# Performance work log

Hardware: AMD Instinct MI355X
Metric: run time of the kernel (lower is better)

Reference implementation:

```python
import jax, jax.numpy as jnp
import numpy as np

SOS = 1

def setup_inputs() -> dict:
    key = jax.random.key(0)
    ks = jax.random.split(key, 12)
    B, S, T, H, V = 64, 128, 32, 1024, 32000
    sc = 0.02
    return {
        'encoder_outputs': jax.random.normal(ks[0], (B, S, H), jnp.float32),
        'encoder_hidden': jax.random.normal(ks[1], (1, B, H), jnp.float32),
        'target_tensor': jax.random.randint(ks[2], (B, T), 0, V),
        'embedding': jax.random.normal(ks[3], (V, H), jnp.float32) * sc,
        'Wa': jax.random.normal(ks[4], (H, H), jnp.float32) * sc,
        'ba': jnp.zeros((H,), jnp.float32),
        'Ua': jax.random.normal(ks[5], (H, H), jnp.float32) * sc,
        'bu': jnp.zeros((H,), jnp.float32),
        'Va': jax.random.normal(ks[6], (1, H), jnp.float32) * sc,
        'bv': jnp.zeros((1,), jnp.float32),
        'W_ih': jax.random.normal(ks[7], (3 * H, 2 * H), jnp.float32) * sc,
        'b_ih': jnp.zeros((3 * H,), jnp.float32),
        'W_hh': jax.random.normal(ks[8], (3 * H, H), jnp.float32) * sc,
        'b_hh': jnp.zeros((3 * H,), jnp.float32),
        'W_out': jax.random.normal(ks[9], (V, H), jnp.float32) * sc,
        'b_out': jnp.zeros((V,), jnp.float32),
    }

def reference(encoder_outputs, encoder_hidden, target_tensor, embedding,
              Wa, ba, Ua, bu, Va, bv, W_ih, b_ih, W_hh, b_hh, W_out, b_out):
    B, S, H = encoder_outputs.shape
    T = target_tensor.shape[1]
    # teacher forcing: input at step i is SOS for i=0 else target[:, i-1]
    tokens = jnp.concatenate([jnp.full((B, 1), SOS, target_tensor.dtype),
                              target_tensor[:, :-1]], axis=1)  # (B,T)
    emb = embedding[tokens]  # (B,T,H); dropout is identity (eval)
    keys_proj = jnp.einsum('bsh,gh->bsg', encoder_outputs, Ua) + bu  # Ua(keys), (B,S,H)
    h0 = encoder_hidden[0]  # (B,H)

    def step(h, x_t):
        # Bahdanau attention: Va(tanh(Wa q + Ua k))
        q = h @ Wa.T + ba  # (B,H)
        scores = jnp.einsum('bsh,h->bs', jnp.tanh(q[:, None, :] + keys_proj), Va[0]) + bv[0]
        w = jax.nn.softmax(scores, axis=-1)  # (B,S)
        ctx = jnp.einsum('bs,bsh->bh', w, encoder_outputs)
        x = jnp.concatenate([x_t, ctx], axis=-1)  # (B,2H)
        # GRU cell (PyTorch convention)
        gi = x @ W_ih.T + b_ih
        gh = h @ W_hh.T + b_hh
        ir, iz, inn = jnp.split(gi, 3, axis=-1)
        hr, hz, hn = jnp.split(gh, 3, axis=-1)
        r = jax.nn.sigmoid(ir + hr)
        z = jax.nn.sigmoid(iz + hz)
        n = jnp.tanh(inn + r * hn)
        h_new = (1.0 - z) * n + z * h
        logits = h_new @ W_out.T + b_out  # (B,V)
        return h_new, (logits, w)

    h_final, (logits, weights) = jax.lax.scan(step, h0, jnp.swapaxes(emb, 0, 1))
    log_probs = jax.nn.log_softmax(jnp.swapaxes(logits, 0, 1), axis=-1)  # (B,T,V)
    attentions = jnp.swapaxes(weights, 0, 1)  # (B,T,S)
    return log_probs, h_final[None], attentions
```

## Files before the change

### kernel.cpp

```cpp
#include <hip/hip_runtime.h>


typedef unsigned short u16;
typedef __bf16 bf16x8 __attribute__((ext_vector_type(8)));
typedef float f32x4 __attribute__((ext_vector_type(4)));
typedef u16 u16x8 __attribute__((ext_vector_type(8)));

#define DEV __device__ __forceinline__

DEV u16 f2b(float f) {
  union { float f; unsigned u; } v; v.f = f;
  unsigned r = v.u + 0x7fffu + ((v.u >> 16) & 1u);
  return (u16)(r >> 16);
}
DEV float b2f(u16 b) {
  union { unsigned u; float f; } v; v.u = ((unsigned)b) << 16;
  return v.f;
}
DEV float sigm(float x) { return 1.f / (1.f + __expf(-x)); }
DEV float ftanh(float x) {
  x = fminf(fmaxf(x, -20.f), 20.f);
  float e = __expf(2.f * x);
  return (e - 1.f) / (e + 1.f);
}
DEV void gl16(const void* g, void* l) {
  __builtin_amdgcn_global_load_lds((const __attribute__((address_space(1))) void*)g,
                                   (__attribute__((address_space(3))) void*)l, 16, 0, 0);
}

__global__ __launch_bounds__(256) void cvtall(const float* __restrict__ enc, const float* __restrict__ Ua,
                                              const float* __restrict__ Wa, const float* __restrict__ Whh,
                                              const float* __restrict__ Wout, u16* __restrict__ enc_b,
                                              u16* __restrict__ Ua_b, u16* __restrict__ Wa_b,
                                              u16* __restrict__ Whh_b, u16* __restrict__ Wout_b) {
  const long q_enc = 2097152;
  const long q_ua = q_enc + 262144;
  const long q_wa = q_ua + 262144;
  const long q_whh = q_wa + 786432;
  const long total = q_whh + 8192000;
  long stride = (long)gridDim.x * 256;
  for (long i = (long)blockIdx.x * 256 + threadIdx.x; i < total; i += stride) {
    const float* src; u16* dst; long off;
    if (i < q_enc) { src = enc; dst = enc_b; off = i; }
    else if (i < q_ua) { src = Ua; dst = Ua_b; off = i - q_enc; }
    else if (i < q_wa) { src = Wa; dst = Wa_b; off = i - q_ua; }
    else if (i < q_whh) { src = Whh; dst = Whh_b; off = i - q_wa; }
    else { src = Wout; dst = Wout_b; off = i - q_whh; }
    float4 v = ((const float4*)src)[off];
    ushort4 o; o.x = f2b(v.x); o.y = f2b(v.y); o.z = f2b(v.z); o.w = f2b(v.w);
    ((ushort4*)dst)[off] = o;
  }
}

__global__ __launch_bounds__(256) void cvtsplitk(const float* __restrict__ in, u16* __restrict__ o1,
                                                 u16* __restrict__ o2) {
  const long n4 = (long)3072 * 2048 / 4;
  long stride = (long)gridDim.x * 256;
  for (long i = (long)blockIdx.x * 256 + threadIdx.x; i < n4; i += stride) {
    long e = i * 4;
    int row = (int)(e >> 11), col = (int)(e & 2047);
    float4 v = ((const float4*)in)[i];
    ushort4 o; o.x = f2b(v.x); o.y = f2b(v.y); o.z = f2b(v.z); o.w = f2b(v.w);
    u16* dst = (col < 1024) ? (o1 + (size_t)row * 1024 + col) : (o2 + (size_t)row * 1024 + col - 1024);
    *(ushort4*)dst = o;
  }
}

__global__ __launch_bounds__(256) void embk(const float* __restrict__ embd, const int* __restrict__ tgt,
                                            u16* __restrict__ out) {
  int i = blockIdx.x * 256 + threadIdx.x;
  size_t e = (size_t)i * 4;
  int h = (int)(e & 1023);
  int bt = (int)(e >> 10);
  int b = bt >> 5, t = bt & 31;
  int tok = (t == 0) ? 1 : tgt[b * 32 + t - 1];
  const float* src = embd + (size_t)tok * 1024 + h;
  ushort4 o; o.x = f2b(src[0]); o.y = f2b(src[1]); o.z = f2b(src[2]); o.w = f2b(src[3]);
  *(ushort4*)(out + e) = o;
}

__global__ __launch_bounds__(256) void hinitk(const float* __restrict__ eh, float* __restrict__ hf,
                                              u16* __restrict__ hb) {
  int i = blockIdx.x * 256 + threadIdx.x;
  float v = eh[i];
  hf[i] = v; hb[i] = f2b(v);
}

template <int MODE>
__global__ __launch_bounds__(256) void gemm_tile(const u16* __restrict__ A, const u16* __restrict__ Bm,
                                                 const float* __restrict__ bias, float* __restrict__ Cf,
                                                 u16* __restrict__ Cb, int K, int ldc, int nTM) {
  __shared__ __attribute__((aligned(16))) u16 As[128 * 32];
  __shared__ __attribute__((aligned(16))) u16 Bs[128 * 32];
  const int tid = threadIdx.x, lane = tid & 63, w = tid >> 6;
  const int chunk = gridDim.x >> 3, wg = blockIdx.x;
  const int id = (wg & 7) * chunk + (wg >> 3);
  const int m = id % nTM, n = id / nTM;
  const int m0 = m * 128, n0 = n * 128;
  const int wm = w >> 1, wn = w & 1;
  const int l16 = lane & 15, kg = lane >> 4;
  const int srow = lane >> 2;
  const int skk = (((lane & 3) ^ ((srow >> 1) & 3)) * 8);
  const int slot = (kg ^ ((l16 >> 1) & 3)) * 8;

  f32x4 acc[4][4];
#pragma unroll
  for (int i = 0; i < 4; ++i)
#pragma unroll
    for (int j = 0; j < 4; ++j) acc[i][j] = f32x4{0.f, 0.f, 0.f, 0.f};

  for (int k0 = 0; k0 < K; k0 += 32) {
#pragma unroll
    for (int ch = 0; ch < 2; ++ch) {
      int c = w + ch * 4;
      gl16(A + (size_t)(m0 + c * 16 + srow) * K + k0 + skk, &As[c * 512]);
      gl16(Bm + (size_t)(n0 + c * 16 + srow) * K + k0 + skk, &Bs[c * 512]);
    }
    __syncthreads();
    bf16x8 av[4], bv[4];
#pragma unroll
    for (int i = 0; i < 4; ++i) av[i] = *(const bf16x8*)&As[(wm * 4 + i) * 512 + l16 * 32 + slot];
#pragma unroll
    for (int j = 0; j < 4; ++j) bv[j] = *(const bf16x8*)&Bs[(wn * 4 + j) * 512 + l16 * 32 + slot];
#pragma unroll
    for (int i = 0; i < 4; ++i)
#pragma unroll
      for (int j = 0; j < 4; ++j)
        acc[i][j] = __builtin_amdgcn_mfma_f32_16x16x32_bf16(av[i], bv[j], acc[i][j], 0, 0, 0);
    __syncthreads();
  }
#pragma unroll
  for (int i = 0; i < 4; ++i) {
    int rowb = m0 + (wm * 4 + i) * 16 + kg * 4;
#pragma unroll
    for (int j = 0; j < 4; ++j) {
      int col = n0 + (wn * 4 + j) * 16 + l16;
      float bb = bias[col];
#pragma unroll
      for (int r = 0; r < 4; ++r) {
        int row = rowb + r;
        float v = acc[i][j][r] + bb;
        if (MODE == 0) Cf[(size_t)row * ldc + col] = v;
        else Cb[(size_t)row * ldc + col] = f2b(v);
      }
    }
  }
}

template <int MODE>
__global__ __launch_bounds__(256, 2) void gemm_wide(const u16* __restrict__ A, const u16* __restrict__ Bm,
                                                    const float* __restrict__ bias, float* __restrict__ Cf,
                                                    u16* __restrict__ Cb, int K, int ldc) {
  __shared__ __attribute__((aligned(16))) u16 As[128 * 32];
  __shared__ __attribute__((aligned(16))) u16 Bs[256 * 32];
  const int tid = threadIdx.x, lane = tid & 63, w = tid >> 6;
  const int chunk = gridDim.x >> 3, wg = blockIdx.x;
  const int id = (wg & 7) * chunk + (wg >> 3);
  const int r_ = id % 80;
  const int m = r_ & 15, n = 5 * (id / 80) + (r_ >> 4);
  const int m0 = m * 128, n0 = n * 256;
  const int wm = w >> 1, wn = w & 1;
  const int l16 = lane & 15, kg = lane >> 4;
  const int srow = lane >> 2;
  const int skk = (((lane & 3) ^ ((srow >> 1) & 3)) * 8);
  const int slot = (kg ^ ((l16 >> 1) & 3)) * 8;

  f32x4 acc[4][8];
#pragma unroll
  for (int i = 0; i < 4; ++i)
#pragma unroll
    for (int j = 0; j < 8; ++j) acc[i][j] = f32x4{0.f, 0.f, 0.f, 0.f};

  for (int k0 = 0; k0 < K; k0 += 32) {
#pragma unroll
    for (int ch = 0; ch < 2; ++ch) {
      int c = w + ch * 4;
      gl16(A + (size_t)(m0 + c * 16 + srow) * K + k0 + skk, &As[c * 512]);
    }
#pragma unroll
    for (int ch = 0; ch < 4; ++ch) {
      int c = w + ch * 4;
      gl16(Bm + (size_t)(n0 + c * 16 + srow) * K + k0 + skk, &Bs[c * 512]);
    }
    __syncthreads();
    bf16x8 av[4], bv[8];
#pragma unroll
    for (int i = 0; i < 4; ++i) av[i] = *(const bf16x8*)&As[(wm * 4 + i) * 512 + l16 * 32 + slot];
#pragma unroll
    for (int j = 0; j < 8; ++j) bv[j] = *(const bf16x8*)&Bs[(wn * 8 + j) * 512 + l16 * 32 + slot];
#pragma unroll
    for (int i = 0; i < 4; ++i)
#pragma unroll
      for (int j = 0; j < 8; ++j)
        acc[i][j] = __builtin_amdgcn_mfma_f32_16x16x32_bf16(av[i], bv[j], acc[i][j], 0, 0, 0);
    __syncthreads();
  }
#pragma unroll
  for (int i = 0; i < 4; ++i) {
    int rowb = m0 + (wm * 4 + i) * 16 + kg * 4;
#pragma unroll
    for (int j = 0; j < 8; ++j) {
      int col = n0 + (wn * 8 + j) * 16 + l16;
      float bb = bias[col];
#pragma unroll
      for (int r = 0; r < 4; ++r) {
        int row = rowb + r;
        float v = acc[i][j][r] + bb;
        int b_ = row & 63, t_ = row >> 6;
        size_t ro = ((size_t)b_ * 32 + t_) * ldc + col;
        if (MODE == 0) Cf[ro] = v; else Cb[ro] = f2b(v);
      }
    }
  }
}

__global__ __launch_bounds__(256) void qkghk(const u16* __restrict__ hb, const u16* __restrict__ W1,
                                             float* __restrict__ qghp) {
  const int tid = threadIdx.x, lane = tid & 63, w = tid >> 6;
  const int l16 = lane & 15, kg = lane >> 4;
  const int pg = blockIdx.x >> 2, ks = blockIdx.x & 3;
  const u16* ap = hb + (size_t)(w * 16 + l16) * 1024 + ks * 256 + kg * 8;
  const u16* bp = W1 + (size_t)(pg * 16 + l16) * 1024 + ks * 256 + kg * 8;
  f32x4 a = {0.f, 0.f, 0.f, 0.f};
#pragma unroll
  for (int k0 = 0; k0 < 256; k0 += 32)
    a = __builtin_amdgcn_mfma_f32_16x16x32_bf16(*(const bf16x8*)(ap + k0), *(const bf16x8*)(bp + k0),
                                                a, 0, 0, 0);
  const int col = pg * 16 + l16;
#pragma unroll
  for (int r = 0; r < 4; ++r) {
    int b = w * 16 + kg * 4 + r;
    qghp[(size_t)ks * 262144 + b * 4096 + col] = a[r];
  }
}

__global__ __launch_bounds__(256) void scorekq(const float* __restrict__ qghp, const float* __restrict__ ba,
                                               const float* __restrict__ Va, const u16* __restrict__ kp,
                                               float* __restrict__ sc) {
  const int b = blockIdx.x >> 2, sq = blockIdx.x & 3;
  const int tid = threadIdx.x, lane = tid & 63, w = tid >> 6;
  __shared__ float qs[1024], vas[1024];
#pragma unroll
  for (int j = 0; j < 4; ++j) {
    int e = tid + j * 256;
    qs[e] = qghp[b * 4096 + e] + qghp[262144 + b * 4096 + e] + qghp[524288 + b * 4096 + e] +
            qghp[786432 + b * 4096 + e] + ba[e];
    vas[e] = Va[e];
  }
  __syncthreads();
#pragma unroll
  for (int si = 0; si < 8; ++si) {
    int s = sq * 32 + w * 8 + si;
    const bf16x8* kv = (const bf16x8*)(kp + ((size_t)b * 128 + s) * 1024);
    float a = 0.f;
#pragma unroll
    for (int i2 = 0; i2 < 2; ++i2) {
      int e = lane + 64 * i2;
      bf16x8 k8 = kv[e];
#pragma unroll
      for (int j = 0; j < 8; ++j) a += vas[e * 8 + j] * ftanh(qs[e * 8 + j] + (float)k8[j]);
    }
#pragma unroll
    for (int off = 32; off; off >>= 1) a += __shfl_xor(a, off);
    if (lane == 0) sc[b * 128 + s] = a;
  }
}

__global__ __launch_bounds__(256) void wsumgate(const float* __restrict__ scb, const u16* __restrict__ encW2,
                                                const float* __restrict__ gie, const float* __restrict__ qghp,
                                                const float* __restrict__ bhh, float* __restrict__ hf,
                                                u16* __restrict__ hbW, u16* __restrict__ hall,
                                                float* __restrict__ hfin, float* __restrict__ att_out, int t) {
  const int b = blockIdx.x >> 2, cg = blockIdx.x & 3;
  const int tid = threadIdx.x, lane = tid & 63, w = tid >> 6;
  __shared__ float wsm[128];
  if (w == 0) {
    float v0 = scb[b * 128 + lane], v1 = scb[b * 128 + 64 + lane];
    float mx = fmaxf(v0, v1);
#pragma unroll
    for (int off = 32; off; off >>= 1) mx = fmaxf(mx, __shfl_xor(mx, off));
    float e0 = __expf(v0 - mx), e1 = __expf(v1 - mx);
    float sm = e0 + e1;
#pragma unroll
    for (int off = 32; off; off >>= 1) sm += __shfl_xor(sm, off);
    float inv = 1.f / sm;
    e0 *= inv; e1 *= inv;
    wsm[lane] = e0; wsm[lane + 64] = e1;
    if (cg == 0) {
      size_t ao = ((size_t)b * 32 + t) * 128;
      att_out[ao + lane] = e0;
      att_out[ao + lane + 64] = e1;
    }
  }
  __syncthreads();
  const int col = cg * 256 + tid;
  float a0 = 0.f, a1 = 0.f, a2 = 0.f;
  const u16* ep = encW2 + (size_t)b * 128 * 3072 + col;
#pragma unroll 8
  for (int s = 0; s < 128; ++s) {
    float ws = wsm[s];
    a0 += ws * b2f(ep[0]);
    a1 += ws * b2f(ep[1024]);
    a2 += ws * b2f(ep[2048]);
    ep += 3072;
  }
  const float* ge = gie + ((size_t)b * 32 + t) * 3072 + col;
  const float* qg = qghp + (size_t)b * 4096 + 1024 + col;
  float hr = qg[0] + qg[262144] + qg[524288] + qg[786432] + bhh[col];
  float hz = qg[1024] + qg[1024 + 262144] + qg[1024 + 524288] + qg[1024 + 786432] + bhh[col + 1024];
  float hn = qg[2048] + qg[2048 + 262144] + qg[2048 + 524288] + qg[2048 + 786432] + bhh[col + 2048];
  float rr = sigm(a0 + ge[0] + hr);
  float zz = sigm(a1 + ge[1024] + hz);
  float nn = ftanh(a2 + ge[2048] + rr * hn);
  const int i = b * 1024 + col;
  float hp = hf[i];
  float hv = (1.f - zz) * nn + zz * hp;
  hf[i] = hv;
  u16 h16 = f2b(hv);
  hbW[i] = h16;
  hall[((size_t)t * 64 + b) * 1024 + col] = h16;
  if (t == 31) hfin[i] = hv;
}

__global__ __launch_bounds__(256) void smaxctxk(const float* __restrict__ sc, const u16* __restrict__ encb,
                                                u16* __restrict__ ctxb, float* __restrict__ att_out, int t) {
  const int b = blockIdx.x >> 2, hq = blockIdx.x & 3;
  const int tid = threadIdx.x, lane = tid & 63, w = tid >> 6;
  __shared__ float wsm[128];
  if (w == 0) {
    float v0 = sc[b * 128 + lane], v1 = sc[b * 128 + 64 + lane];
    float mx = fmaxf(v0, v1);
#pragma unroll
    for (int off = 32; off; off >>= 1) mx = fmaxf(mx, __shfl_xor(mx, off));
    float e0 = __expf(v0 - mx), e1 = __expf(v1 - mx);
    float sm = e0 + e1;
#pragma unroll
    for (int off = 32; off; off >>= 1) sm += __shfl_xor(sm, off);
    float inv = 1.f / sm;
    e0 *= inv; e1 *= inv;
    wsm[lane] = e0; wsm[lane + 64] = e1;
    if (hq == 0) {
      size_t ao = ((size_t)b * 32 + t) * 128;
      att_out[ao + lane] = e0;
      att_out[ao + lane + 64] = e1;
    }
  }
  __syncthreads();
  const int h = hq * 256 + tid;
  const u16* ep = encb + (size_t)b * 131072 + h;
  float c = 0.f;
#pragma unroll 8
  for (int s = 0; s < 128; ++s) c += wsm[s] * b2f(ep[(size_t)s * 1024]);
  ctxb[(size_t)b * 1024 + h] = f2b(c);
}

__global__ __launch_bounds__(256) void gi2w(const u16* __restrict__ ctxb, const u16* __restrict__ Wih2,
                                            float* __restrict__ gic) {
  const int tid = threadIdx.x, lane = tid & 63, w = tid >> 6;
  const int l16 = lane & 15, kg = lane >> 4;
  const int c0 = blockIdx.x * 16;
  const u16* ap = ctxb + (size_t)(w * 16 + l16) * 1024 + kg * 8;
  const u16* bp = Wih2 + (size_t)(c0 + l16) * 1024 + kg * 8;
  f32x4 a0 = {0.f, 0.f, 0.f, 0.f}, a1 = {0.f, 0.f, 0.f, 0.f};
#pragma unroll 4
  for (int k0 = 0; k0 < 1024; k0 += 64) {
    a0 = __builtin_amdgcn_mfma_f32_16x16x32_bf16(*(const bf16x8*)(ap + k0), *(const bf16x8*)(bp + k0),
                                                 a0, 0, 0, 0);
    a1 = __builtin_amdgcn_mfma_f32_16x16x32_bf16(*(const bf16x8*)(ap + k0 + 32),
                                                 *(const bf16x8*)(bp + k0 + 32), a1, 0, 0, 0);
  }
  const int col = c0 + l16;
#pragma unroll
  for (int r = 0; r < 4; ++r) {
    int b = w * 16 + kg * 4 + r;
    gic[(size_t)b * 3072 + col] = a0[r] + a1[r];
  }
}

__global__ __launch_bounds__(256) void gatesq(const float* __restrict__ gic, const float* __restrict__ gie,
                                              const float* __restrict__ qghp, const float* __restrict__ bhh,
                                              float* __restrict__ hf, u16* __restrict__ hbW,
                                              u16* __restrict__ hall, float* __restrict__ hfin, int t) {
  const int i = blockIdx.x * 256 + threadIdx.x;
  const int b = i >> 10, col = i & 1023;
  const float* gi = gic + (size_t)b * 3072 + col;
  const float* ge = gie + ((size_t)b * 32 + t) * 3072 + col;
  const float* qg = qghp + (size_t)b * 4096 + 1024 + col;
  float hr = qg[0] + qg[262144] + qg[524288] + qg[786432] + bhh[col];
  float hz = qg[1024] + qg[1024 + 262144] + qg[1024 + 524288] + qg[1024 + 786432] + bhh[col + 1024];
  float hn = qg[2048] + qg[2048 + 262144] + qg[2048 + 524288] + qg[2048 + 786432] + bhh[col + 2048];
  float rr = sigm(gi[0] + ge[0] + hr);
  float zz = sigm(gi[1024] + ge[1024] + hz);
  float nn = ftanh(gi[2048] + ge[2048] + rr * hn);
  float hp = hf[i];
  float hv = (1.f - zz) * nn + zz * hp;
  hf[i] = hv;
  u16 h16 = f2b(hv);
  hbW[i] = h16;
  hall[((size_t)t * 64 + b) * 1024 + col] = h16;
  if (t == 31) hfin[i] = hv;
}

__global__ __launch_bounds__(256) void logsoftk(const u16* __restrict__ lg, float* __restrict__ out) {
  const int row = blockIdx.x, tid = threadIdx.x, lane = tid & 63, w = tid >> 6;
  const u16x8* p = (const u16x8*)(lg + (size_t)row * 32000);
  __shared__ float red[4];
  u16x8 d[16];
#pragma unroll
  for (int j = 0; j < 16; ++j) {
    int i = tid + j * 256;
    if (i < 4000) d[j] = p[i];
  }
  float mx = -3.0e38f;
#pragma unroll
  for (int j = 0; j < 16; ++j) {
    int i = tid + j * 256;
    if (i < 4000)
#pragma unroll
      for (int k = 0; k < 8; ++k) mx = fmaxf(mx, b2f(d[j][k]));
  }
#pragma unroll
  for (int off = 32; off; off >>= 1) mx = fmaxf(mx, __shfl_xor(mx, off));
  if (lane == 0) red[w] = mx;
  __syncthreads();
  mx = fmaxf(fmaxf(red[0], red[1]), fmaxf(red[2], red[3]));
  __syncthreads();
  float s = 0.f;
#pragma unroll
  for (int j = 0; j < 16; ++j) {
    int i = tid + j * 256;
    if (i < 4000)
#pragma unroll
      for (int k = 0; k < 8; ++k) s += __expf(b2f(d[j][k]) - mx);
  }
#pragma unroll
  for (int off = 32; off; off >>= 1) s += __shfl_xor(s, off);
  if (lane == 0) red[w] = s;
  __syncthreads();
  float c = mx + __logf(red[0] + red[1] + red[2] + red[3]);
  float* op = out + (size_t)row * 32000;
#pragma unroll
  for (int j = 0; j < 16; ++j) {
    int i = tid + j * 256;
    if (i < 4000) {
      f32x4 o0, o1;
#pragma unroll
      for (int k = 0; k < 4; ++k) { o0[k] = b2f(d[j][k]) - c; o1[k] = b2f(d[j][k + 4]) - c; }
      *(f32x4*)(op + i * 8) = o0;
      *(f32x4*)(op + i * 8 + 4) = o1;
    }
  }
}

__global__ __launch_bounds__(256) void rowstatk(const float* __restrict__ lp, float* __restrict__ c) {
  int row = blockIdx.x;
  const float4* p = (const float4*)(lp + (size_t)row * 32000);
  int tid = threadIdx.x, lane = tid & 63, w = tid >> 6;
  __shared__ float redm[4], reds[4];
  float mx = -3.0e38f;
  for (int i = tid; i < 8000; i += 256) {
    float4 v = p[i];
    mx = fmaxf(mx, fmaxf(fmaxf(v.x, v.y), fmaxf(v.z, v.w)));
  }
#pragma unroll
  for (int off = 32; off; off >>= 1) mx = fmaxf(mx, __shfl_xor(mx, off));
  if (lane == 0) redm[w] = mx;
  __syncthreads();
  mx = fmaxf(fmaxf(redm[0], redm[1]), fmaxf(redm[2], redm[3]));
  float s = 0.f;
  for (int i = tid; i < 8000; i += 256) {
    float4 v = p[i];
    s += __expf(v.x - mx) + __expf(v.y - mx) + __expf(v.z - mx) + __expf(v.w - mx);
  }
#pragma unroll
  for (int off = 32; off; off >>= 1) s += __shfl_xor(s, off);
  if (lane == 0) reds[w] = s;
  __syncthreads();
  if (tid == 0) c[row] = mx + __logf(reds[0] + reds[1] + reds[2] + reds[3]);
}

__global__ __launch_bounds__(256) void subk(float* __restrict__ lp, const float* __restrict__ c) {
  const long n4 = (long)64 * 32 * 32000 / 4;
  long stride = (long)gridDim.x * 256;
  for (long i = (long)blockIdx.x * 256 + threadIdx.x; i < n4; i += stride) {
    float4 v = ((float4*)lp)[i];
    float cc = c[i / 8000];
    v.x -= cc; v.y -= cc; v.z -= cc; v.w -= cc;
    ((float4*)lp)[i] = v;
  }
}

extern "C" void kernel_launch(void* const* d_in, const int* in_sizes, int n_in, void* d_out, int out_size,
                              void* d_ws, size_t ws_size, hipStream_t stream) {
  (void)in_sizes; (void)n_in; (void)out_size;
  constexpr int B = 64, S = 128, T = 32, H = 1024, V = 32000;

  const float* enc  = (const float*)d_in[0];
  const float* ehid = (const float*)d_in[1];
  const int*   tgt  = (const int*)d_in[2];
  const float* embd = (const float*)d_in[3];
  const float* Wa   = (const float*)d_in[4];
  const float* ba   = (const float*)d_in[5];
  const float* Ua   = (const float*)d_in[6];
  const float* bu   = (const float*)d_in[7];
  const float* Va   = (const float*)d_in[8];
  const float* Wih  = (const float*)d_in[10];
  const float* bih  = (const float*)d_in[11];
  const float* Whh  = (const float*)d_in[12];
  const float* bhh  = (const float*)d_in[13];
  const float* Wout = (const float*)d_in[14];
  const float* bout = (const float*)d_in[15];

  char* wp = (char*)d_ws;
  auto alloc = [&](size_t bytes) {
    char* p = wp;
    wp += (bytes + 255) & ~(size_t)255;
    return p;
  };
  u16* enc_b  = (u16*)alloc((size_t)B * S * H * 2);
  u16* kp_b   = (u16*)alloc((size_t)B * S * H * 2);
  u16* Ua_b   = (u16*)alloc((size_t)H * H * 2);
  u16* W1_b   = (u16*)alloc((size_t)4096 * 1024 * 2);
  u16* Wih1_b = (u16*)alloc((size_t)3072 * 1024 * 2);
  u16* Wih2_b = (u16*)alloc((size_t)3072 * 1024 * 2);
  u16* Wout_b = (u16*)alloc((size_t)V * H * 2);
  u16* emb_b  = (u16*)alloc((size_t)B * T * H * 2);
  u16* hall_b = (u16*)alloc((size_t)T * B * H * 2);
  float* gie  = (float*)alloc((size_t)B * T * 3072 * 4);
  float* qghp = (float*)alloc((size_t)4 * B * 4096 * 4);
  float* scb  = (float*)alloc((size_t)B * S * 4);
  float* gic  = (float*)alloc((size_t)B * 3072 * 4);
  u16* ctx_b  = (u16*)alloc((size_t)B * H * 2);
  u16* hb0    = (u16*)alloc((size_t)B * H * 2);
  u16* hb1    = (u16*)alloc((size_t)B * H * 2);
  float* h_f  = (float*)alloc((size_t)B * H * 4);
  float* rowc = (float*)alloc(2048 * 4);
  float* zbias = (float*)alloc(3072 * 4);
  size_t base_need = (size_t)(wp - (char*)d_ws);
  u16* encW2 = (u16*)alloc((size_t)B * S * 3072 * 2);
  bool have_w2 = ((size_t)(wp - (char*)d_ws) <= ws_size);
  u16* lg_b = (u16*)alloc((size_t)B * T * V * 2);
  bool bflog = ((size_t)(wp - (char*)d_ws) <= ws_size);
  if (base_need > ws_size) return;

  float* out_lp = (float*)d_out;
  float* out_hf = out_lp + (size_t)B * T * V;
  float* out_at = out_hf + (size_t)B * H;

  u16* Wa_slot = W1_b;
  u16* Whh_slot = W1_b + (size_t)1024 * 1024;
  cvtall<<<2048, 256, 0, stream>>>(enc, Ua, Wa, Whh, Wout, enc_b, Ua_b, Wa_slot, Whh_slot, Wout_b);
  cvtsplitk<<<2048, 256, 0, stream>>>(Wih, Wih1_b, Wih2_b);
  embk<<<2048, 256, 0, stream>>>(embd, tgt, emb_b);
  hinitk<<<256, 256, 0, stream>>>(ehid, h_f, hb0);

  gemm_tile<1><<<512, 256, 0, stream>>>(enc_b, Ua_b, bu, nullptr, kp_b, H, H, 64);
  gemm_tile<0><<<384, 256, 0, stream>>>(emb_b, Wih1_b, bih, gie, nullptr, H, 3072, 16);
  if (have_w2) {
    hipMemsetAsync(zbias, 0, 3072 * 4, stream);
    gemm_tile<1><<<1536, 256, 0, stream>>>(enc_b, Wih2_b, zbias, nullptr, encW2, H, 3072, 64);
  }

  for (int t = 0; t < T; ++t) {
    u16* hbR = (t & 1) ? hb1 : hb0;
    u16* hbW = (t & 1) ? hb0 : hb1;
    qkghk<<<1024, 256, 0, stream>>>(hbR, W1_b, qghp);
    scorekq<<<256, 256, 0, stream>>>(qghp, ba, Va, kp_b, scb);
    if (have_w2) {
      wsumgate<<<256, 256, 0, stream>>>(scb, encW2, gie, qghp, bhh, h_f, hbW, hall_b, out_hf, out_at, t);
    } else {
      smaxctxk<<<256, 256, 0, stream>>>(scb, enc_b, ctx_b, out_at, t);
      gi2w<<<192, 256, 0, stream>>>(ctx_b, Wih2_b, gic);
      gatesq<<<256, 256, 0, stream>>>(gic, gie, qghp, bhh, h_f, hbW, hall_b, out_hf, t);
    }
  }

  if (bflog) {
    gemm_wide<1><<<2000, 256, 0, stream>>>(hall_b, Wout_b, bout, nullptr, lg_b, H, V);
    logsoftk<<<2048, 256, 0, stream>>>(lg_b, out_lp);
  } else {
    gemm_wide<0><<<2000, 256, 0, stream>>>(hall_b, Wout_b, bout, out_lp, nullptr, H, V);
    rowstatk<<<2048, 256, 0, stream>>>(out_lp, rowc);
    subk<<<2048, 256, 0, stream>>>(out_lp, rowc);
  }
}
```

Measured before the change: 1.540 ms.

## Fuse attention scoring into gate kernel and halve split-K in hidden projection

The per-step score kernel is merged into the weighted-sum/GRU-gate kernel, so each block computes all 128 scores for its batch row in shared memory instead of reading them from a global buffer. This removes one launch per timestep. The qkghk projection drops from 4-way to 2-way split-K, which halves the partial-sum reads and the buffer size. In exchange, each of the 4 column-group blocks per batch row now recomputes the full score vector, doing four times the tanh work and key reads, and qkghk launches fewer, longer blocks.

```diff
diff --git a/kernel.cpp b/kernel.cpp
--- a/kernel.cpp
+++ b/kernel.cpp
@@ -218,12 +218,12 @@
                                              float* __restrict__ qghp) {
   const int tid = threadIdx.x, lane = tid & 63, w = tid >> 6;
   const int l16 = lane & 15, kg = lane >> 4;
-  const int pg = blockIdx.x >> 2, ks = blockIdx.x & 3;
-  const u16* ap = hb + (size_t)(w * 16 + l16) * 1024 + ks * 256 + kg * 8;
-  const u16* bp = W1 + (size_t)(pg * 16 + l16) * 1024 + ks * 256 + kg * 8;
+  const int pg = blockIdx.x >> 1, ks = blockIdx.x & 1;
+  const u16* ap = hb + (size_t)(w * 16 + l16) * 1024 + ks * 512 + kg * 8;
+  const u16* bp = W1 + (size_t)(pg * 16 + l16) * 1024 + ks * 512 + kg * 8;
   f32x4 a = {0.f, 0.f, 0.f, 0.f};
 #pragma unroll
-  for (int k0 = 0; k0 < 256; k0 += 32)
+  for (int k0 = 0; k0 < 512; k0 += 32)
     a = __builtin_amdgcn_mfma_f32_16x16x32_bf16(*(const bf16x8*)(ap + k0), *(const bf16x8*)(bp + k0),
                                                 a, 0, 0, 0);
   const int col = pg * 16 + l16;
@@ -234,23 +234,25 @@
   }
 }
 
-__global__ __launch_bounds__(256) void scorekq(const float* __restrict__ qghp, const float* __restrict__ ba,
+__global__ __launch_bounds__(256) void attgate(const float* __restrict__ qghp, const float* __restrict__ ba,
                                                const float* __restrict__ Va, const u16* __restrict__ kp,
-                                               float* __restrict__ sc) {
-  const int b = blockIdx.x >> 2, sq = blockIdx.x & 3;
+                                               const u16* __restrict__ encW2, const float* __restrict__ gie,
+                                               const float* __restrict__ bhh, float* __restrict__ hf,
+                                               u16* __restrict__ hbW, u16* __restrict__ hall,
+                                               float* __restrict__ hfin, float* __restrict__ att_out, int t) {
+  const int b = blockIdx.x >> 2, cg = blockIdx.x & 3;
   const int tid = threadIdx.x, lane = tid & 63, w = tid >> 6;
-  __shared__ float qs[1024], vas[1024];
+  __shared__ float qs[1024], vas[1024], wsm[128];
 #pragma unroll
   for (int j = 0; j < 4; ++j) {
     int e = tid + j * 256;
-    qs[e] = qghp[b * 4096 + e] + qghp[262144 + b * 4096 + e] + qghp[524288 + b * 4096 + e] +
-            qghp[786432 + b * 4096 + e] + ba[e];
+    qs[e] = qghp[b * 4096 + e] + qghp[262144 + b * 4096 + e] + ba[e];
     vas[e] = Va[e];
   }
   __syncthreads();
-#pragma unroll
-  for (int si = 0; si < 8; ++si) {
-    int s = sq * 32 + w * 8 + si;
+#pragma unroll 4
+  for (int si = 0; si < 32; ++si) {
+    int s = w * 32 + si;
     const bf16x8* kv = (const bf16x8*)(kp + ((size_t)b * 128 + s) * 1024);
     float a = 0.f;
 #pragma unroll
@@ -262,20 +264,11 @@
     }
 #pragma unroll
     for (int off = 32; off; off >>= 1) a += __shfl_xor(a, off);
-    if (lane == 0) sc[b * 128 + s] = a;
-  }
-}
-
-__global__ __launch_bounds__(256) void wsumgate(const float* __restrict__ scb, const u16* __restrict__ encW2,
-                                                const float* __restrict__ gie, const float* __restrict__ qghp,
-                                                const float* __restrict__ bhh, float* __restrict__ hf,
-                                                u16* __restrict__ hbW, u16* __restrict__ hall,
-                                                float* __restrict__ hfin, float* __restrict__ att_out, int t) {
-  const int b = blockIdx.x >> 2, cg = blockIdx.x & 3;
-  const int tid = threadIdx.x, lane = tid & 63, w = tid >> 6;
-  __shared__ float wsm[128];
+    if (lane == 0) wsm[s] = a;
+  }
+  __syncthreads();
   if (w == 0) {
-    float v0 = scb[b * 128 + lane], v1 = scb[b * 128 + 64 + lane];
+    float v0 = wsm[lane], v1 = wsm[lane + 64];
     float mx = fmaxf(v0, v1);
 #pragma unroll
     for (int off = 32; off; off >>= 1) mx = fmaxf(mx, __shfl_xor(mx, off));
@@ -306,9 +299,9 @@
   }
   const float* ge = gie + ((size_t)b * 32 + t) * 3072 + col;
   const float* qg = qghp + (size_t)b * 4096 + 1024 + col;
-  float hr = qg[0] + qg[262144] + qg[524288] + qg[786432] + bhh[col];
-  float hz = qg[1024] + qg[1024 + 262144] + qg[1024 + 524288] + qg[1024 + 786432] + bhh[col + 1024];
-  float hn = qg[2048] + qg[2048 + 262144] + qg[2048 + 524288] + qg[2048 + 786432] + bhh[col + 2048];
+  float hr = qg[0] + qg[262144] + bhh[col];
+  float hz = qg[1024] + qg[1024 + 262144] + bhh[col + 1024];
+  float hn = qg[2048] + qg[2048 + 262144] + bhh[col + 2048];
   float rr = sigm(a0 + ge[0] + hr);
   float zz = sigm(a1 + ge[1024] + hz);
   float nn = ftanh(a2 + ge[2048] + rr * hn);
@@ -320,6 +313,37 @@
   hbW[i] = h16;
   hall[((size_t)t * 64 + b) * 1024 + col] = h16;
   if (t == 31) hfin[i] = hv;
+}
+
+__global__ __launch_bounds__(256) void scorekq(const float* __restrict__ qghp, const float* __restrict__ ba,
+                                               const float* __restrict__ Va, const u16* __restrict__ kp,
+                                               float* __restrict__ sc) {
+  const int b = blockIdx.x >> 2, sq = blockIdx.x & 3;
+  const int tid = threadIdx.x, lane = tid & 63, w = tid >> 6;
+  __shared__ float qs[1024], vas[1024];
+#pragma unroll
+  for (int j = 0; j < 4; ++j) {
+    int e = tid + j * 256;
+    qs[e] = qghp[b * 4096 + e] + qghp[262144 + b * 4096 + e] + ba[e];
+    vas[e] = Va[e];
+  }
+  __syncthreads();
+#pragma unroll
+  for (int si = 0; si < 8; ++si) {
+    int s = sq * 32 + w * 8 + si;
+    const bf16x8* kv = (const bf16x8*)(kp + ((size_t)b * 128 + s) * 1024);
+    float a = 0.f;
+#pragma unroll
+    for (int i2 = 0; i2 < 2; ++i2) {
+      int e = lane + 64 * i2;
+      bf16x8 k8 = kv[e];
+#pragma unroll
+      for (int j = 0; j < 8; ++j) a += vas[e * 8 + j] * ftanh(qs[e * 8 + j] + (float)k8[j]);
+    }
+#pragma unroll
+    for (int off = 32; off; off >>= 1) a += __shfl_xor(a, off);
+    if (lane == 0) sc[b * 128 + s] = a;
+  }
 }
 
 __global__ __launch_bounds__(256) void smaxctxk(const float* __restrict__ sc, const u16* __restrict__ encb,
@@ -386,9 +410,9 @@
   const float* gi = gic + (size_t)b * 3072 + col;
   const float* ge = gie + ((size_t)b * 32 + t) * 3072 + col;
   const float* qg = qghp + (size_t)b * 4096 + 1024 + col;
-  float hr = qg[0] + qg[262144] + qg[524288] + qg[786432] + bhh[col];
-  float hz = qg[1024] + qg[1024 + 262144] + qg[1024 + 524288] + qg[1024 + 786432] + bhh[col + 1024];
-  float hn = qg[2048] + qg[2048 + 262144] + qg[2048 + 524288] + qg[2048 + 786432] + bhh[col + 2048];
+  float hr = qg[0] + qg[262144] + bhh[col];
+  float hz = qg[1024] + qg[1024 + 262144] + bhh[col + 1024];
+  float hn = qg[2048] + qg[2048 + 262144] + bhh[col + 2048];
   float rr = sigm(gi[0] + ge[0] + hr);
   float zz = sigm(gi[1024] + ge[1024] + hz);
   float nn = ftanh(gi[2048] + ge[2048] + rr * hn);
@@ -527,7 +551,7 @@
   u16* emb_b  = (u16*)alloc((size_t)B * T * H * 2);
   u16* hall_b = (u16*)alloc((size_t)T * B * H * 2);
   float* gie  = (float*)alloc((size_t)B * T * 3072 * 4);
-  float* qghp = (float*)alloc((size_t)4 * B * 4096 * 4);
+  float* qghp = (float*)alloc((size_t)2 * B * 4096 * 4);
   float* scb  = (float*)alloc((size_t)B * S * 4);
   float* gic  = (float*)alloc((size_t)B * 3072 * 4);
   u16* ctx_b  = (u16*)alloc((size_t)B * H * 2);
@@ -564,11 +588,12 @@
   for (int t = 0; t < T; ++t) {
     u16* hbR = (t & 1) ? hb1 : hb0;
     u16* hbW = (t & 1) ? hb0 : hb1;
-    qkghk<<<1024, 256, 0, stream>>>(hbR, W1_b, qghp);
-    scorekq<<<256, 256, 0, stream>>>(qghp, ba, Va, kp_b, scb);
+    qkghk<<<512, 256, 0, stream>>>(hbR, W1_b, qghp);
     if (have_w2) {
-      wsumgate<<<256, 256, 0, stream>>>(scb, encW2, gie, qghp, bhh, h_f, hbW, hall_b, out_hf, out_at, t);
+      attgate<<<256, 256, 0, stream>>>(qghp, ba, Va, kp_b, encW2, gie, bhh, h_f, hbW, hall_b,
+                                       out_hf, out_at, t);
     } else {
+      scorekq<<<256, 256, 0, stream>>>(qghp, ba, Va, kp_b, scb);
       smaxctxk<<<256, 256, 0, stream>>>(scb, enc_b, ctx_b, out_at, t);
       gi2w<<<192, 256, 0, stream>>>(ctx_b, Wih2_b, gic);
       gatesq<<<256, 256, 0, stream>>>(gic, gie, qghp, bhh, h_f, hbW, hall_b, out_hf, t);
```

After: 2.329 ms. 51.2% more time.
